# Performance work log

Hardware: AMD Instinct MI355X
Metric: run time of the kernel (lower is better)

Reference implementation:

```python
import jax, jax.numpy as jnp
import numpy as np

B, S, E = 1, 2048, 4096
HQ, HKV = 32, 8
D = E // HQ          # 128
RATIO = HQ // HKV    # 4
CACHE = 1024
T = CACHE + S        # 3072


def setup_inputs() -> dict:
    key = jax.random.key(0)
    ks = jax.random.split(key, 8)
    sc = lambda fan_in: 1.0 / np.sqrt(fan_in)
    x = jax.random.normal(ks[0], (B, S, E), dtype=jnp.float32)
    w_q = jax.random.normal(ks[1], (E, E), dtype=jnp.float32) * sc(E)
    w_k = jax.random.normal(ks[2], (E, HKV * D), dtype=jnp.float32) * sc(E)
    w_v = jax.random.normal(ks[3], (E, HKV * D), dtype=jnp.float32) * sc(E)
    w_o = jax.random.normal(ks[4], (E, E), dtype=jnp.float32) * sc(E)
    k_cache = jax.random.normal(ks[5], (B, HKV, CACHE, D), dtype=jnp.float32)
    v_cache = jax.random.normal(ks[6], (B, HKV, CACHE, D), dtype=jnp.float32)
    # causal additive mask with cache offset: query i may attend key j iff j <= i + CACHE
    q_pos = jnp.arange(S)[:, None] + CACHE
    k_pos = jnp.arange(T)[None, :]
    attention_mask = jnp.where(k_pos <= q_pos, 0.0, -1e9).astype(jnp.float32)
    return {"x": x, "w_q": w_q, "w_k": w_k, "w_v": w_v, "w_o": w_o,
            "k_cache": k_cache, "v_cache": v_cache, "attention_mask": attention_mask}


def reference(x, w_q, w_k, w_v, w_o, k_cache, v_cache, attention_mask):
    # Projections, split into heads: [B, H, S, D]
    Q = (x @ w_q).reshape(B, S, HQ, D).transpose(0, 2, 1, 3)
    K_new = (x @ w_k).reshape(B, S, HKV, D).transpose(0, 2, 1, 3)
    V_new = (x @ w_v).reshape(B, S, HKV, D).transpose(0, 2, 1, 3)
    # KV-cache concat along time
    K = jnp.concatenate([k_cache, K_new], axis=2)  # [B, HKV, T, D]
    V = jnp.concatenate([v_cache, V_new], axis=2)
    # GQA grouping as in source: (head group) with group = HKV
    Qg = Q.reshape(B, RATIO, HKV, S, D)            # [B, h, g, S, D]
    scores = jnp.einsum('bhgsd,bgtd->bhgst', Qg, K) / jnp.sqrt(jnp.asarray(D, x.dtype))
    scores = scores + attention_mask               # broadcast [S, T]
    att = jax.nn.softmax(scores, axis=-1)
    res = jnp.einsum('bhgst,bgtd->bhgsd', att, V)  # [B, h, g, S, D]
    # '... head group s dhead -> ... s (head group dhead)'
    res = res.transpose(0, 3, 1, 2, 4).reshape(B, S, E)
    out = res @ w_o
    return (out, (K, V))
```

## Files before the change

kernel.cpp:

```cpp
#include <hip/hip_runtime.h>

typedef unsigned short u16;
typedef unsigned int u32;
typedef __attribute__((ext_vector_type(8))) short short8;
typedef __attribute__((ext_vector_type(4))) float f32x4;

#define S_LEN 2048
#define E_DIM 4096
#define NHQ 32
#define NHKV 8
#define HD 128
#define CACHE_LEN 1024
#define T_LEN 3072
#define KV_ELEMS ((size_t)NHKV * T_LEN * HD)

__device__ __forceinline__ u16 f2bf(float f) {
  union { float f; u32 u; } v; v.f = f;
  u32 u = v.u;
  return (u16)((u + 0x7FFFu + ((u >> 16) & 1u)) >> 16);
}

__device__ __forceinline__ void gl_lds16(const void* g, void* l) {
  __builtin_amdgcn_global_load_lds(
      (const __attribute__((address_space(1))) unsigned int*)g,
      (__attribute__((address_space(3))) unsigned int*)l, 16, 0, 0);
}

__global__ __launch_bounds__(256) void cvt_x(const float* __restrict__ x,
                                             u16* __restrict__ xb) {
  int i = blockIdx.x * 256 + threadIdx.x;
  float4 v = ((const float4*)x)[i];
  uint2 o;
  o.x = (u32)f2bf(v.x) | ((u32)f2bf(v.y) << 16);
  o.y = (u32)f2bf(v.z) | ((u32)f2bf(v.w) << 16);
  ((uint2*)xb)[i] = o;
}

__global__ __launch_bounds__(256) void copy_caches(
    const float4* __restrict__ kc, const float4* __restrict__ vc,
    float4* __restrict__ Ko, float4* __restrict__ Vo,
    uint2* __restrict__ Kb) {
  int i = blockIdx.x * 256 + threadIdx.x;
  int h = i >> 15;
  size_t o = (size_t)i + ((size_t)h << 16);
  float4 v = kc[i];
  Ko[o] = v;
  uint2 b;
  b.x = (u32)f2bf(v.x) | ((u32)f2bf(v.y) << 16);
  b.y = (u32)f2bf(v.z) | ((u32)f2bf(v.w) << 16);
  Kb[o] = b;
  Vo[o] = vc[i];
}

__global__ __launch_bounds__(256) void cvt_vcT(const float* __restrict__ vc,
                                               u16* __restrict__ vbT) {
  __shared__ u16 t[64][68];
  const int tid = threadIdx.x;
  const int h = blockIdx.z;
  const int t0 = blockIdx.x << 6;
  const int d0 = blockIdx.y << 6;
  const float* in = vc + ((size_t)h * CACHE_LEN + t0) * HD + d0;
  const int rl = tid >> 4;
  const int c4 = (tid & 15) << 2;
#pragma unroll
  for (int i = 0; i < 4; ++i) {
    int rr = rl + (i << 4);
    float4 v = *(const float4*)&in[(size_t)rr * HD + c4];
    t[c4 + 0][rr] = f2bf(v.x);
    t[c4 + 1][rr] = f2bf(v.y);
    t[c4 + 2][rr] = f2bf(v.z);
    t[c4 + 3][rr] = f2bf(v.w);
  }
  __syncthreads();
  u16* outp = vbT + ((size_t)h * HD + d0) * T_LEN + t0;
#pragma unroll
  for (int p = 0; p < 2; ++p) {
    int idx = tid + (p << 8);
    int dr = idx >> 3;
    int ch = (idx & 7) << 3;
    u32 a0 = (u32)t[dr][ch + 0] | ((u32)t[dr][ch + 1] << 16);
    u32 a1 = (u32)t[dr][ch + 2] | ((u32)t[dr][ch + 3] << 16);
    u32 a2 = (u32)t[dr][ch + 4] | ((u32)t[dr][ch + 5] << 16);
    u32 a3 = (u32)t[dr][ch + 6] | ((u32)t[dr][ch + 7] << 16);
    uint4 o4; o4.x = a0; o4.y = a1; o4.z = a2; o4.w = a3;
    *(uint4*)&outp[(size_t)dr * T_LEN + ch] = o4;
  }
}

__global__ __launch_bounds__(256) void cvt_wt(const float* __restrict__ w,
                                              u16* __restrict__ wt,
                                              int K, int N) {
  __shared__ u16 t[64][68];
  const int tid = threadIdx.x;
  const int ntk = K >> 6;
  const int k0 = (blockIdx.x % ntk) << 6;
  const int n0 = (blockIdx.x / ntk) << 6;
  const int kl = tid >> 4;
  const int nl4 = (tid & 15) << 2;
#pragma unroll
  for (int i = 0; i < 4; ++i) {
    int kk = kl + (i << 4);
    float4 v = *(const float4*)&w[(size_t)(k0 + kk) * N + n0 + nl4];
    t[nl4 + 0][kk] = f2bf(v.x);
    t[nl4 + 1][kk] = f2bf(v.y);
    t[nl4 + 2][kk] = f2bf(v.z);
    t[nl4 + 3][kk] = f2bf(v.w);
  }
  __syncthreads();
  const int onl = tid >> 3;
  const int okc = (tid & 7) << 3;
#pragma unroll
  for (int p = 0; p < 2; ++p) {
    int nl = onl + (p << 5);
    u32 a0 = (u32)t[nl][okc + 0] | ((u32)t[nl][okc + 1] << 16);
    u32 a1 = (u32)t[nl][okc + 2] | ((u32)t[nl][okc + 3] << 16);
    u32 a2 = (u32)t[nl][okc + 4] | ((u32)t[nl][okc + 5] << 16);
    u32 a3 = (u32)t[nl][okc + 6] | ((u32)t[nl][okc + 7] << 16);
    uint4 o4; o4.x = a0; o4.y = a1; o4.z = a2; o4.w = a3;
    *(uint4*)&wt[(size_t)(n0 + nl) * K + k0 + okc] = o4;
  }
}

template<int MODE>
__global__ __launch_bounds__(256) void gemm2(
    const u16* __restrict__ A, const u16* __restrict__ Bt,
    int M, int N, int K,
    float* __restrict__ outF, u16* __restrict__ outB, u16* __restrict__ outB2) {
  __shared__ __align__(16) u16 Als[128 * 32];
  __shared__ __align__(16) u16 Bls[128 * 32];
  const int tid = threadIdx.x;
  const int lane = tid & 63;
  const int wave = tid >> 6;
  const int wr = wave >> 1, wc = wave & 1;
  const int l15 = lane & 15, l4 = lane >> 4;
  const int nbn = N >> 7;
  const int bm0 = (blockIdx.x / nbn) << 7;
  const int bn0 = (blockIdx.x % nbn) << 7;

  f32x4 acc[4][4];
#pragma unroll
  for (int i = 0; i < 4; ++i)
#pragma unroll
    for (int j = 0; j < 4; ++j) {
      acc[i][j][0] = 0.f; acc[i][j][1] = 0.f;
      acc[i][j][2] = 0.f; acc[i][j][3] = 0.f;
    }

  const u16* Abase = A + (size_t)bm0 * K;
  const u16* Bbase = Bt + (size_t)bn0 * K;
  const int c0 = tid, c1 = tid + 256;
  const int r0 = c0 >> 2, q0c = (c0 & 3) << 3;
  const int r1 = c1 >> 2, q1c = (c1 & 3) << 3;

  for (int k0 = 0; k0 < K; k0 += 32) {
    __syncthreads();
    gl_lds16(Abase + (size_t)r0 * K + k0 + q0c, &Als[c0 << 3]);
    gl_lds16(Bbase + (size_t)r0 * K + k0 + q0c, &Bls[c0 << 3]);
    gl_lds16(Abase + (size_t)r1 * K + k0 + q1c, &Als[c1 << 3]);
    gl_lds16(Bbase + (size_t)r1 * K + k0 + q1c, &Bls[c1 << 3]);
    __syncthreads();

    short8 af[4], bfr[4];
#pragma unroll
    for (int mi = 0; mi < 4; ++mi)
      af[mi] = *(const short8*)&Als[((wr << 6) + (mi << 4) + l15) * 32 + (l4 << 3)];
#pragma unroll
    for (int ni = 0; ni < 4; ++ni)
      bfr[ni] = *(const short8*)&Bls[((wc << 6) + (ni << 4) + l15) * 32 + (l4 << 3)];
#pragma unroll
    for (int mi = 0; mi < 4; ++mi)
#pragma unroll
      for (int ni = 0; ni < 4; ++ni)
        acc[mi][ni] = __builtin_amdgcn_mfma_f32_16x16x32_bf16(af[mi], bfr[ni],
                                                              acc[mi][ni], 0, 0, 0);
  }
#pragma unroll
  for (int mi = 0; mi < 4; ++mi) {
#pragma unroll
    for (int ni = 0; ni < 4; ++ni) {
#pragma unroll
      for (int r = 0; r < 4; ++r) {
        int row = bm0 + (wr << 6) + (mi << 4) + (l4 << 2) + r;
        int col = bn0 + (wc << 6) + (ni << 4) + l15;
        float v = acc[mi][ni][r];
        if (MODE == 0) {
          outB[(size_t)row * N + col] = f2bf(v);
        } else if (MODE == 1) {
          int hv = col >> 7;
          int d = col & 127;
          int h = hv & 7;
          if (hv < 8) {
            size_t idx = ((size_t)h * T_LEN + (CACHE_LEN + row)) * HD + d;
            outF[idx] = v;
            outB[idx] = f2bf(v);
          } else {
            size_t idxF = ((size_t)h * T_LEN + (CACHE_LEN + row)) * HD + d + KV_ELEMS;
            outF[idxF] = v;
            outB2[((size_t)h * HD + d) * T_LEN + (CACHE_LEN + row)] = f2bf(v);
          }
        } else {
          outF[(size_t)row * N + col] = v;
        }
      }
    }
  }
}

__global__ __launch_bounds__(512, 2) void attn_fwd(
    const u16* __restrict__ Qb, const u16* __restrict__ Kb,
    const u16* __restrict__ VbT, u16* __restrict__ resB) {
  __shared__ __align__(16) u16 Kls[2][64 * 128];
  __shared__ __align__(16) u16 Vls[2][128 * 64];
  __shared__ __align__(16) u16 Pls[8][16][72];
  const int tid = threadIdx.x;
  const int lane = tid & 63;
  const int wave = tid >> 6;
  const int l15 = lane & 15, l4 = lane >> 4;
  const int bid = blockIdx.x;
  const int hq = bid & 31;
  const int bx = bid >> 5;
  const int kvh = hq & 7;
  const int q0 = bx << 8;
  const int qw = q0 + (wave << 5);

  short8 aq[2][4];
#pragma unroll
  for (int rg = 0; rg < 2; ++rg) {
    const u16* qrow = Qb + (size_t)(qw + (rg << 4) + l15) * E_DIM + hq * HD;
#pragma unroll
    for (int kd = 0; kd < 4; ++kd)
      aq[rg][kd] = *(const short8*)(qrow + (kd << 5) + (l4 << 3));
  }

  f32x4 accO[2][8];
  float mrow[2][4], lrow[2][4];
#pragma unroll
  for (int rg = 0; rg < 2; ++rg) {
#pragma unroll
    for (int nd = 0; nd < 8; ++nd) {
      accO[rg][nd][0] = 0.f; accO[rg][nd][1] = 0.f;
      accO[rg][nd][2] = 0.f; accO[rg][nd][3] = 0.f;
    }
#pragma unroll
    for (int r = 0; r < 4; ++r) { mrow[rg][r] = -1e30f; lrow[rg][r] = 0.f; }
  }

  const u16* Kh = Kb + (size_t)kvh * T_LEN * HD;
  const u16* VTh = VbT + (size_t)kvh * (size_t)HD * T_LEN;
  const int nt = (bx << 2) + 20;

  const int trk = (wave << 3) + (lane >> 4);
  const int jd0 = (lane & 15) ^ (trk & 7);
  const int jd1 = (lane & 15) ^ ((trk + 4) & 7);
  const u16* kp0 = Kh + (size_t)trk * HD + (jd0 << 3);
  const u16* kp1 = Kh + (size_t)(trk + 4) * HD + (jd1 << 3);
  const int drv = (wave << 4) + (lane >> 3);
  const int tj0 = (lane & 7) ^ (drv & 7);
  const u16* vp0 = VTh + (size_t)drv * T_LEN + (tj0 << 3);
  const u16* vp1 = VTh + (size_t)(drv + 8) * T_LEN + (tj0 << 3);

#define STAGE(BUF)                                             \
  {                                                            \
    gl_lds16(kp0, &Kls[BUF][((wave << 1) + 0) << 9]);          \
    gl_lds16(kp1, &Kls[BUF][((wave << 1) + 1) << 9]);          \
    gl_lds16(vp0, &Vls[BUF][((wave << 1) + 0) << 9]);          \
    gl_lds16(vp1, &Vls[BUF][((wave << 1) + 1) << 9]);          \
    kp0 += 64 * HD; kp1 += 64 * HD; vp0 += 64; vp1 += 64;      \
  }

  STAGE(0);
  __syncthreads();

  const float scale = 0.08838834764831845f;
  const int xr = (l15 & 7) << 3;

  for (int it = 0; it < nt; ++it) {
    const int cur = it & 1;
    const int t0 = it << 6;
    if (it + 1 < nt) STAGE(cur ^ 1);

    const u16* Kc = &Kls[cur][0];
    const u16* Vc = &Vls[cur][0];

#pragma unroll
    for (int rg = 0; rg < 2; ++rg) {
      const int qrg = qw + (rg << 4);
      float p[4][4];
#pragma unroll
      for (int ct = 0; ct < 4; ++ct) {
        f32x4 sc;
        sc[0] = 0.f; sc[1] = 0.f; sc[2] = 0.f; sc[3] = 0.f;
#pragma unroll
        for (int kd = 0; kd < 4; ++kd) {
          short8 bk = *(const short8*)&Kc[((ct << 4) + l15) * 128 +
                                          (((kd << 5) + (l4 << 3)) ^ xr)];
          sc = __builtin_amdgcn_mfma_f32_16x16x32_bf16(aq[rg][kd], bk, sc, 0, 0, 0);
        }
#pragma unroll
        for (int r = 0; r < 4; ++r) p[ct][r] = sc[r] * scale;
      }

      if ((t0 + 63) > (qrg + CACHE_LEN)) {
#pragma unroll
        for (int ct = 0; ct < 4; ++ct)
#pragma unroll
          for (int r = 0; r < 4; ++r) {
            int qq = qrg + (l4 << 2) + r + CACHE_LEN;
            if (t0 + (ct << 4) + l15 > qq) p[ct][r] = -1e30f;
          }
      }

      float mx[4];
#pragma unroll
      for (int r = 0; r < 4; ++r) {
        float m = fmaxf(fmaxf(p[0][r], p[1][r]), fmaxf(p[2][r], p[3][r]));
        m = fmaxf(m, __shfl_xor(m, 1));
        m = fmaxf(m, __shfl_xor(m, 2));
        m = fmaxf(m, __shfl_xor(m, 4));
        m = fmaxf(m, __shfl_xor(m, 8));
        mx[r] = m;
      }
      bool grow = false;
#pragma unroll
      for (int r = 0; r < 4; ++r) grow = grow || (mx[r] > mrow[rg][r] + 8.f);
      if (__any(grow)) {
#pragma unroll
        for (int r = 0; r < 4; ++r) {
          float mn = fmaxf(mrow[rg][r], mx[r]);
          float corr = __expf(mrow[rg][r] - mn);
          mrow[rg][r] = mn;
          lrow[rg][r] *= corr;
#pragma unroll
          for (int nd = 0; nd < 8; ++nd) accO[rg][nd][r] *= corr;
        }
      }
#pragma unroll
      for (int r = 0; r < 4; ++r) {
        float rs = 0.f;
#pragma unroll
        for (int ct = 0; ct < 4; ++ct) {
          p[ct][r] = __expf(p[ct][r] - mrow[rg][r]);
          rs += p[ct][r];
        }
        rs += __shfl_xor(rs, 1);
        rs += __shfl_xor(rs, 2);
        rs += __shfl_xor(rs, 4);
        rs += __shfl_xor(rs, 8);
        lrow[rg][r] += rs;
      }

#pragma unroll
      for (int ct = 0; ct < 4; ++ct)
#pragma unroll
        for (int r = 0; r < 4; ++r)
          Pls[wave][(l4 << 2) + r][(ct << 4) + l15] = f2bf(p[ct][r]);
      short8 pa0 = *(const short8*)&Pls[wave][l15][l4 << 3];
      short8 pa1 = *(const short8*)&Pls[wave][l15][32 + (l4 << 3)];

#pragma unroll
      for (int nd = 0; nd < 8; ++nd) {
        short8 bv0 = *(const short8*)&Vc[((nd << 4) + l15) * 64 + ((l4 << 3) ^ xr)];
        accO[rg][nd] = __builtin_amdgcn_mfma_f32_16x16x32_bf16(pa0, bv0, accO[rg][nd], 0, 0, 0);
        short8 bv1 = *(const short8*)&Vc[((nd << 4) + l15) * 64 + ((32 + (l4 << 3)) ^ xr)];
        accO[rg][nd] = __builtin_amdgcn_mfma_f32_16x16x32_bf16(pa1, bv1, accO[rg][nd], 0, 0, 0);
      }
    }
    __syncthreads();
  }
#undef STAGE

#pragma unroll
  for (int rg = 0; rg < 2; ++rg) {
    float inv[4];
#pragma unroll
    for (int r = 0; r < 4; ++r) inv[r] = 1.0f / lrow[rg][r];
#pragma unroll
    for (int nd = 0; nd < 8; ++nd) {
#pragma unroll
      for (int r = 0; r < 4; ++r) {
        float v = accO[rg][nd][r] * inv[r];
        int q = qw + (rg << 4) + (l4 << 2) + r;
        int d = (nd << 4) + l15;
        resB[(size_t)q * E_DIM + hq * HD + d] = f2bf(v);
      }
    }
  }
}

extern "C" void kernel_launch(void* const* d_in, const int* in_sizes, int n_in,
                              void* d_out, int out_size, void* d_ws, size_t ws_size,
                              hipStream_t stream) {
  const float* x = (const float*)d_in[0];
  const float* w_q = (const float*)d_in[1];
  const float* w_k = (const float*)d_in[2];
  const float* w_v = (const float*)d_in[3];
  const float* w_o = (const float*)d_in[4];
  const float* k_cache = (const float*)d_in[5];
  const float* v_cache = (const float*)d_in[6];

  float* out = (float*)d_out;
  float* Kout = out + (size_t)S_LEN * E_DIM;

  char* ws = (char*)d_ws;
  const size_t MB = 1024 * 1024;
  u16* xb   = (u16*)(ws);
  u16* resB = (u16*)(ws);
  u16* Qb   = (u16*)(ws + 16 * MB);
  u16* Kb   = (u16*)(ws + 32 * MB);
  u16* VbT  = (u16*)(ws + 38 * MB);
  u16* wkvt = (u16*)(ws + 48 * MB);
  u16* wbig = (u16*)(ws + 64 * MB);

  cvt_x<<<dim3(8192), dim3(256), 0, stream>>>(x, xb);
  copy_caches<<<dim3(1024), dim3(256), 0, stream>>>(
      (const float4*)k_cache, (const float4*)v_cache,
      (float4*)Kout, (float4*)(Kout + KV_ELEMS), (uint2*)Kb);
  cvt_vcT<<<dim3(16, 2, 8), dim3(256), 0, stream>>>(v_cache, VbT);
  cvt_wt<<<dim3(1024), dim3(256), 0, stream>>>(w_k, wkvt, E_DIM, NHKV * HD);
  cvt_wt<<<dim3(1024), dim3(256), 0, stream>>>(w_v, wkvt + (size_t)1024 * E_DIM, E_DIM, NHKV * HD);
  cvt_wt<<<dim3(4096), dim3(256), 0, stream>>>(w_q, wbig, E_DIM, E_DIM);
  gemm2<1><<<dim3(16 * 16), dim3(256), 0, stream>>>(xb, wkvt, S_LEN, 2048, E_DIM, Kout, Kb, VbT);
  gemm2<0><<<dim3(16 * 32), dim3(256), 0, stream>>>(xb, wbig, S_LEN, E_DIM, E_DIM, nullptr, Qb, nullptr);
  cvt_wt<<<dim3(4096), dim3(256), 0, stream>>>(w_o, wbig, E_DIM, E_DIM);
  attn_fwd<<<dim3(256), dim3(512), 0, stream>>>(Qb, Kb, VbT, resB);
  gemm2<2><<<dim3(16 * 32), dim3(256), 0, stream>>>(resB, wbig, S_LEN, E_DIM, E_DIM, out, nullptr, nullptr);
}
```

Measured before the change: 754.8 us.

## Balance causal attention work by pairing light and heavy query tiles per block

Each block now handles two 128-row query tiles, tile pr and tile 15-pr, one after the other, so every block runs the same number of KV iterations. Before, a block owned one 256-row tile and the causal mask made its work vary widely. Each wave now owns 16 query rows instead of 32, so each staged K/V tile is reused over fewer rows and there are more barriers per useful MFMA. The softmax also switches to exp2 with log2(e) folded into the scale, and the rescale threshold is raised to match base-2 units. The P scratch row padding goes from 72 to 74, which makes the row stride 148 bytes, so the 16-byte LDS vector reads are no longer naturally aligned.

```diff
diff --git a/kernel.cpp b/kernel.cpp
--- a/kernel.cpp
+++ b/kernel.cpp
@@ -211,53 +211,26 @@
     const u16* __restrict__ VbT, u16* __restrict__ resB) {
   __shared__ __align__(16) u16 Kls[2][64 * 128];
   __shared__ __align__(16) u16 Vls[2][128 * 64];
-  __shared__ __align__(16) u16 Pls[8][16][72];
+  __shared__ __align__(16) u16 Pls[8][16][74];
   const int tid = threadIdx.x;
   const int lane = tid & 63;
   const int wave = tid >> 6;
   const int l15 = lane & 15, l4 = lane >> 4;
   const int bid = blockIdx.x;
   const int hq = bid & 31;
-  const int bx = bid >> 5;
+  const int pr = bid >> 5;
   const int kvh = hq & 7;
-  const int q0 = bx << 8;
-  const int qw = q0 + (wave << 5);
-
-  short8 aq[2][4];
-#pragma unroll
-  for (int rg = 0; rg < 2; ++rg) {
-    const u16* qrow = Qb + (size_t)(qw + (rg << 4) + l15) * E_DIM + hq * HD;
-#pragma unroll
-    for (int kd = 0; kd < 4; ++kd)
-      aq[rg][kd] = *(const short8*)(qrow + (kd << 5) + (l4 << 3));
-  }
-
-  f32x4 accO[2][8];
-  float mrow[2][4], lrow[2][4];
-#pragma unroll
-  for (int rg = 0; rg < 2; ++rg) {
-#pragma unroll
-    for (int nd = 0; nd < 8; ++nd) {
-      accO[rg][nd][0] = 0.f; accO[rg][nd][1] = 0.f;
-      accO[rg][nd][2] = 0.f; accO[rg][nd][3] = 0.f;
-    }
-#pragma unroll
-    for (int r = 0; r < 4; ++r) { mrow[rg][r] = -1e30f; lrow[rg][r] = 0.f; }
-  }
 
   const u16* Kh = Kb + (size_t)kvh * T_LEN * HD;
   const u16* VTh = VbT + (size_t)kvh * (size_t)HD * T_LEN;
-  const int nt = (bx << 2) + 20;
 
   const int trk = (wave << 3) + (lane >> 4);
   const int jd0 = (lane & 15) ^ (trk & 7);
   const int jd1 = (lane & 15) ^ ((trk + 4) & 7);
-  const u16* kp0 = Kh + (size_t)trk * HD + (jd0 << 3);
-  const u16* kp1 = Kh + (size_t)(trk + 4) * HD + (jd1 << 3);
   const int drv = (wave << 4) + (lane >> 3);
   const int tj0 = (lane & 7) ^ (drv & 7);
-  const u16* vp0 = VTh + (size_t)drv * T_LEN + (tj0 << 3);
-  const u16* vp1 = VTh + (size_t)(drv + 8) * T_LEN + (tj0 << 3);
+  const int xr = (l15 & 7) << 3;
+  const float scale2 = 0.12754245006340912f;
 
 #define STAGE(BUF)                                             \
   {                                                            \
@@ -268,23 +241,44 @@
     kp0 += 64 * HD; kp1 += 64 * HD; vp0 += 64; vp1 += 64;      \
   }
 
-  STAGE(0);
-  __syncthreads();
-
-  const float scale = 0.08838834764831845f;
-  const int xr = (l15 & 7) << 3;
-
-  for (int it = 0; it < nt; ++it) {
-    const int cur = it & 1;
-    const int t0 = it << 6;
-    if (it + 1 < nt) STAGE(cur ^ 1);
-
-    const u16* Kc = &Kls[cur][0];
-    const u16* Vc = &Vls[cur][0];
-
-#pragma unroll
-    for (int rg = 0; rg < 2; ++rg) {
-      const int qrg = qw + (rg << 4);
+  for (int ph = 0; ph < 2; ++ph) {
+    const int qt = ph ? (15 - pr) : pr;
+    const int q0 = qt << 7;
+    const int qw = q0 + (wave << 4);
+    const int nt = (qt << 1) + 18;
+
+    short8 aq[4];
+    const u16* qrow = Qb + (size_t)(qw + l15) * E_DIM + hq * HD;
+#pragma unroll
+    for (int kd = 0; kd < 4; ++kd)
+      aq[kd] = *(const short8*)(qrow + (kd << 5) + (l4 << 3));
+
+    f32x4 accO[8];
+    float mrow[4], lrow[4];
+#pragma unroll
+    for (int nd = 0; nd < 8; ++nd) {
+      accO[nd][0] = 0.f; accO[nd][1] = 0.f;
+      accO[nd][2] = 0.f; accO[nd][3] = 0.f;
+    }
+#pragma unroll
+    for (int r = 0; r < 4; ++r) { mrow[r] = -1e30f; lrow[r] = 0.f; }
+
+    const u16* kp0 = Kh + (size_t)trk * HD + (jd0 << 3);
+    const u16* kp1 = Kh + (size_t)(trk + 4) * HD + (jd1 << 3);
+    const u16* vp0 = VTh + (size_t)drv * T_LEN + (tj0 << 3);
+    const u16* vp1 = VTh + (size_t)(drv + 8) * T_LEN + (tj0 << 3);
+
+    STAGE(0);
+    __syncthreads();
+
+    for (int it = 0; it < nt; ++it) {
+      const int cur = it & 1;
+      const int t0 = it << 6;
+      if (it + 1 < nt) STAGE(cur ^ 1);
+
+      const u16* Kc = &Kls[cur][0];
+      const u16* Vc = &Vls[cur][0];
+
       float p[4][4];
 #pragma unroll
       for (int ct = 0; ct < 4; ++ct) {
@@ -294,18 +288,18 @@
         for (int kd = 0; kd < 4; ++kd) {
           short8 bk = *(const short8*)&Kc[((ct << 4) + l15) * 128 +
                                           (((kd << 5) + (l4 << 3)) ^ xr)];
-          sc = __builtin_amdgcn_mfma_f32_16x16x32_bf16(aq[rg][kd], bk, sc, 0, 0, 0);
+          sc = __builtin_amdgcn_mfma_f32_16x16x32_bf16(aq[kd], bk, sc, 0, 0, 0);
         }
 #pragma unroll
-        for (int r = 0; r < 4; ++r) p[ct][r] = sc[r] * scale;
-      }
-
-      if ((t0 + 63) > (qrg + CACHE_LEN)) {
+        for (int r = 0; r < 4; ++r) p[ct][r] = sc[r] * scale2;
+      }
+
+      if ((t0 + 63) > (qw + CACHE_LEN)) {
 #pragma unroll
         for (int ct = 0; ct < 4; ++ct)
 #pragma unroll
           for (int r = 0; r < 4; ++r) {
-            int qq = qrg + (l4 << 2) + r + CACHE_LEN;
+            int qq = qw + (l4 << 2) + r + CACHE_LEN;
             if (t0 + (ct << 4) + l15 > qq) p[ct][r] = -1e30f;
           }
       }
@@ -322,16 +316,16 @@
       }
       bool grow = false;
 #pragma unroll
-      for (int r = 0; r < 4; ++r) grow = grow || (mx[r] > mrow[rg][r] + 8.f);
+      for (int r = 0; r < 4; ++r) grow = grow || (mx[r] > mrow[r] + 11.0f);
       if (__any(grow)) {
 #pragma unroll
         for (int r = 0; r < 4; ++r) {
-          float mn = fmaxf(mrow[rg][r], mx[r]);
-          float corr = __expf(mrow[rg][r] - mn);
-          mrow[rg][r] = mn;
-          lrow[rg][r] *= corr;
-#pragma unroll
-          for (int nd = 0; nd < 8; ++nd) accO[rg][nd][r] *= corr;
+          float mn = fmaxf(mrow[r], mx[r]);
+          float corr = exp2f(mrow[r] - mn);
+          mrow[r] = mn;
+          lrow[r] *= corr;
+#pragma unroll
+          for (int nd = 0; nd < 8; ++nd) accO[nd][r] *= corr;
         }
       }
 #pragma unroll
@@ -339,14 +333,14 @@
         float rs = 0.f;
 #pragma unroll
         for (int ct = 0; ct < 4; ++ct) {
-          p[ct][r] = __expf(p[ct][r] - mrow[rg][r]);
+          p[ct][r] = exp2f(p[ct][r] - mrow[r]);
           rs += p[ct][r];
         }
         rs += __shfl_xor(rs, 1);
         rs += __shfl_xor(rs, 2);
         rs += __shfl_xor(rs, 4);
         rs += __shfl_xor(rs, 8);
-        lrow[rg][r] += rs;
+        lrow[r] += rs;
       }
 
 #pragma unroll
@@ -360,31 +354,28 @@
 #pragma unroll
       for (int nd = 0; nd < 8; ++nd) {
         short8 bv0 = *(const short8*)&Vc[((nd << 4) + l15) * 64 + ((l4 << 3) ^ xr)];
-        accO[rg][nd] = __builtin_amdgcn_mfma_f32_16x16x32_bf16(pa0, bv0, accO[rg][nd], 0, 0, 0);
+        accO[nd] = __builtin_amdgcn_mfma_f32_16x16x32_bf16(pa0, bv0, accO[nd], 0, 0, 0);
         short8 bv1 = *(const short8*)&Vc[((nd << 4) + l15) * 64 + ((32 + (l4 << 3)) ^ xr)];
-        accO[rg][nd] = __builtin_amdgcn_mfma_f32_16x16x32_bf16(pa1, bv1, accO[rg][nd], 0, 0, 0);
-      }
+        accO[nd] = __builtin_amdgcn_mfma_f32_16x16x32_bf16(pa1, bv1, accO[nd], 0, 0, 0);
+      }
+      __syncthreads();
     }
-    __syncthreads();
-  }
-#undef STAGE
-
-#pragma unroll
-  for (int rg = 0; rg < 2; ++rg) {
+
     float inv[4];
 #pragma unroll
-    for (int r = 0; r < 4; ++r) inv[r] = 1.0f / lrow[rg][r];
+    for (int r = 0; r < 4; ++r) inv[r] = 1.0f / lrow[r];
 #pragma unroll
     for (int nd = 0; nd < 8; ++nd) {
 #pragma unroll
       for (int r = 0; r < 4; ++r) {
-        float v = accO[rg][nd][r] * inv[r];
-        int q = qw + (rg << 4) + (l4 << 2) + r;
+        float v = accO[nd][r] * inv[r];
+        int q = qw + (l4 << 2) + r;
         int d = (nd << 4) + l15;
         resB[(size_t)q * E_DIM + hq * HD + d] = f2bf(v);
       }
     }
   }
+#undef STAGE
 }
 
 extern "C" void kernel_launch(void* const* d_in, const int* in_sizes, int n_in,
```

Measured after the change: 721.2 us. 4.5% less time.
